# Performance work log

Hardware: AMD Instinct MI355X
Metric: run time of the kernel (lower is better)

The kernel has to match this reference:

```python
import jax, jax.numpy as jnp
import numpy as np

EPS = 1e-8

def squash(t, axis=-1):
    sq = jnp.sum(t * t, axis=axis, keepdims=True)
    scale = sq / (1.0 + sq)
    return scale * t / jnp.sqrt(sq + EPS)

def setup_inputs() -> dict:
    key = jax.random.key(0)
    k1, k2 = jax.random.split(key)
    B, N_IN, D_IN, N_OUT, D_OUT = 256, 1152, 8, 10, 16
    x = jax.random.normal(k1, (B, N_IN, D_IN), dtype=jnp.float32)
    W = 0.01 * jax.random.normal(k2, (1, N_IN, N_OUT, D_OUT, D_IN), dtype=jnp.float32)
    return {"x": x, "W": W}

def reference(x, W):
    # u_hat[b,n,o,j] = sum_i W[0,n,o,j,i] * x[b,n,i]   -> (B, N_in, N_out, D_out)
    u_hat = jnp.einsum('noji,bni->bnoj', W[0], x)
    # b_ij starts with batch dim 1 (as in original torch code) and broadcasts
    b_ij = jnp.zeros((1, u_hat.shape[1], u_hat.shape[2], 1), dtype=u_hat.dtype)
    v_j = None
    for _ in range(3):  # fixed 3 routing iterations
        c_ij = jax.nn.softmax(b_ij, axis=2)            # over output capsules
        s_j = jnp.sum(c_ij * u_hat, axis=1, keepdims=True)  # (B,1,N_out,D_out)
        v_j = squash(s_j, axis=-1)
        b_ij = b_ij + jnp.sum(u_hat * v_j, axis=-1, keepdims=True)
    return jnp.squeeze(v_j, axis=1)  # (B, N_out, D_out)
```

## Files before the change

### kernel.cpp

```cpp
#include <hip/hip_runtime.h>

#define B_ 256
#define N_IN 1152
#define N_OUT 10
#define D_OUT 16
#define OJ 160
#define SN (B_*OJ)
#define LOG2E 1.44269504088896340736f
#define NPB 16
#define NPW 4
#define NSG (N_IN/NPB)
#define NPASSB (NSG*16)

typedef __attribute__((ext_vector_type(8))) short bf16x8;
typedef __attribute__((ext_vector_type(4))) float f32x4;

#define NW_ELEMS (N_IN*N_OUT*D_OUT)
#define NX_ELEMS (B_*N_IN)
#define NWB (NW_ELEMS/256)
#define NTILES ((N_IN/16)*(B_/16))

__device__ __forceinline__ unsigned short f2bf(float f) {
  unsigned u = __float_as_uint(f);
  u += 0x7fffu + ((u >> 16) & 1u);
  return (unsigned short)(u >> 16);
}
__device__ __forceinline__ float bf2f(unsigned short s) {
  return __uint_as_float(((unsigned)s) << 16);
}
__device__ __forceinline__ void split8(const float* p, bf16x8& vh, bf16x8& vl) {
  const float4 a = *(const float4*)p;
  const float4 b = *(const float4*)(p + 4);
  const float w[8] = {a.x,a.y,a.z,a.w,b.x,b.y,b.z,b.w};
#pragma unroll
  for (int e=0;e<8;e++){
    unsigned short hh = f2bf(w[e]);
    vh[e] = (short)hh;
    vl[e] = (short)f2bf(w[e] - bf2f(hh));
  }
}

template<int CTRL>
__device__ __forceinline__ float dpp_add(float xx) {
  int y = __builtin_amdgcn_mov_dpp(__float_as_int(xx), CTRL, 0xF, 0xF, false);
  return xx + __int_as_float(y);
}
__device__ __forceinline__ float row_sum16(float xx) {
  xx = dpp_add<0x128>(xx); xx = dpp_add<0x124>(xx);
  xx = dpp_add<0x122>(xx); xx = dpp_add<0x121>(xx);
  return xx;
}
__device__ __forceinline__ float squash_elem(float t) {
  const float sq = row_sum16(t * t);
  return t * (sq / (1.f + sq)) * rsqrtf(sq + 1e-8f);
}

__device__ __forceinline__ void sgbg_map(int bid, int& sg, int& bg) {
  const int xcd = bid & 7, q = bid >> 3;
  sg = xcd*9 + (q % 9);
  bg = q / 9;
}

__global__ __launch_bounds__(256) void pack_all(const float* __restrict__ W,
                                                const float* __restrict__ x,
                                                short* __restrict__ WH, short* __restrict__ WL,
                                                short* __restrict__ XH, short* __restrict__ XL) {
  const int bid = blockIdx.x, tid = threadIdx.x;
  if (bid < NWB) {
    const int t = bid*256 + tid;
    bf16x8 vh, vl; split8(W + (size_t)t*8, vh, vl);
    ((bf16x8*)WH)[t] = vh; ((bf16x8*)WL)[t] = vl;
  } else {
    __shared__ bf16x8 TH[16*17], TL[16*17];
    const int tile = bid - NWB;
    const int nt = tile >> 4, bt = tile & 15;
    const int nn = tid & 15, bb = tid >> 4;
    bf16x8 vh, vl;
    split8(x + ((size_t)(bt*16+bb)*N_IN + nt*16+nn)*8, vh, vl);
    TH[nn*17 + bb] = vh; TL[nn*17 + bb] = vl;
    __syncthreads();
    const int bb2 = tid & 15, nn2 = tid >> 4;
    const size_t o = (size_t)(nt*16+nn2)*B_ + bt*16 + bb2;
    ((bf16x8*)XH)[o] = TH[nn2*17 + bb2];
    ((bf16x8*)XL)[o] = TL[nn2*17 + bb2];
  }
}


__global__ __launch_bounds__(256) void caps_pass1(const short* __restrict__ WH,
                                                  const short* __restrict__ WL,
                                                  const short* __restrict__ XH,
                                                  const short* __restrict__ XL,
                                                  float* __restrict__ P) {
  __shared__ f32x4 red[3*640];
  int sg, bg; sgbg_map(blockIdx.x, sg, bg);
  const int tid = threadIdx.x, w = tid >> 6, l = tid & 63;
  const int bb = l & 15, c = l >> 4;
  const int b0 = bg * 16;
  const int n0 = sg * NPB + w * NPW;
  const short* Abase = (c & 1)  ? WL : WH;
  const short* Bbase = (c >> 1) ? XL : XH;

  f32x4 acc[N_OUT];
  const f32x4 zz = {0.f,0.f,0.f,0.f};
#pragma unroll
  for (int o=0;o<N_OUT;o++) acc[o] = zz;

  for (int nn=0; nn<NPW; ++nn) {
    const int n = n0 + nn;
    const bf16x8 bfrag = *(const bf16x8*)&Bbase[((size_t)n*B_ + b0 + bb)*8];
    const short* Ap = &Abase[(size_t)n*1280 + bb*8];
#pragma unroll
    for (int o=0;o<N_OUT;o++) {
      const bf16x8 afrag = *(const bf16x8*)&Ap[o*128];
      acc[o] = __builtin_amdgcn_mfma_f32_16x16x32_bf16(afrag, bfrag, acc[o], 0,0,0);
    }
  }

  if (w) {
#pragma unroll
    for (int o=0;o<N_OUT;o++) red[(w-1)*640 + o*64 + l] = acc[o];
  }
  __syncthreads();
  if (!w) {
    float* Pp = &P[(size_t)sg*SN + (size_t)(b0 + bb)*OJ + c*4];
#pragma unroll
    for (int o=0;o<N_OUT;o++) {
      acc[o] += red[o*64+l] + red[640+o*64+l] + red[1280+o*64+l];
      *(f32x4*)&Pp[o*16] = acc[o];
    }
  }
}

__global__ __launch_bounds__(256) void caps_pass23(const short* __restrict__ WH,
                                                   const short* __restrict__ WL,
                                                   const short* __restrict__ XH,
                                                   const short* __restrict__ XL,
                                                   const float* __restrict__ veff,
                                                   float* __restrict__ P) {
  __shared__ f32x4 red[3*640];
  int sg, bg; sgbg_map(blockIdx.x, sg, bg);
  const int tid = threadIdx.x, w = tid >> 6, l = tid & 63;
  const int bb = l & 15, c = l >> 4;
  const int b0 = bg * 16;
  const int n0 = sg * NPB + w * NPW;
  const short* Abase = (c & 1)  ? WL : WH;
  const short* Bbase = (c >> 1) ? XL : XH;

  f32x4 vj[N_OUT], acc[N_OUT];
  const f32x4 zz = {0.f,0.f,0.f,0.f};
  const float* vp = &veff[(size_t)(b0+bb)*OJ + c*4];
#pragma unroll
  for (int o=0;o<N_OUT;o++) { vj[o] = *(const f32x4*)&vp[o*16]; acc[o] = zz; }

  for (int nn=0; nn<NPW; ++nn) {
    const int n = n0 + nn;
    const bf16x8 bfrag = *(const bf16x8*)&Bbase[((size_t)n*B_ + b0 + bb)*8];
    const short* Ap = &Abase[(size_t)n*1280 + bb*8];
    f32x4 u[N_OUT];
#pragma unroll
    for (int o=0;o<N_OUT;o++) {
      const bf16x8 afrag = *(const bf16x8*)&Ap[o*128];
      u[o] = __builtin_amdgcn_mfma_f32_16x16x32_bf16(afrag, bfrag, zz, 0,0,0);
    }
    float ez[N_OUT], Z = 0.f;
#pragma unroll
    for (int o=0;o<N_OUT;o++) {
      float t = u[o][0]*vj[o][0] + u[o][1]*vj[o][1]
              + u[o][2]*vj[o][2] + u[o][3]*vj[o][3];
      t += __shfl_xor(t, 16);
      t += __shfl_xor(t, 32);
      ez[o] = exp2f(t);
      Z += ez[o];
    }
    const float invZ = __builtin_amdgcn_rcpf(Z);
#pragma unroll
    for (int o=0;o<N_OUT;o++) acc[o] += (ez[o] * invZ) * u[o];
  }

  if (w) {
#pragma unroll
    for (int o=0;o<N_OUT;o++) red[(w-1)*640 + o*64 + l] = acc[o];
  }
  __syncthreads();
  if (!w) {
    float* Pp = &P[(size_t)sg*SN + (size_t)(b0 + bb)*OJ + c*4];
#pragma unroll
    for (int o=0;o<N_OUT;o++) {
      acc[o] += red[o*64+l] + red[640+o*64+l] + red[1280+o*64+l];
      *(f32x4*)&Pp[o*16] = acc[o];
    }
  }
}

__global__ __launch_bounds__(256) void caps_finish(const float* __restrict__ P, float scale,
                                                   const float* __restrict__ vprev,
                                                   float* __restrict__ vout, float lscale) {
  const int idx = blockIdx.x*256 + threadIdx.x;
  float t = 0.f;
#pragma unroll 8
  for (int g=0; g<NSG; ++g) t += P[(size_t)g*SN + idx];
  t *= scale;
  float v = squash_elem(t) * lscale;
  if (vprev != nullptr) v += vprev[idx];
  vout[idx] = v;
}

extern "C" void kernel_launch(void* const* d_in, const int* in_sizes, int n_in,
                              void* d_out, int out_size, void* d_ws, size_t ws_size,
                              hipStream_t stream) {
  const float* x = (const float*)d_in[0];
  const float* W = (const float*)d_in[1];
  float* out = (float*)d_out;

  float* P   = (float*)d_ws;
  float* v1  = P  + (size_t)NSG*SN;
  float* v12 = v1 + SN;
  short* WH = (short*)(v12 + SN);
  short* WL = WH + (size_t)NW_ELEMS*8;
  short* XH = WL + (size_t)NW_ELEMS*8;
  short* XL = XH + (size_t)NX_ELEMS*8;

  pack_all<<<NWB + NTILES, 256, 0, stream>>>(W, x, WH, WL, XH, XL);

  caps_pass1<<<NPASSB, 256, 0, stream>>>(WH, WL, XH, XL, P);
  caps_finish<<<SN/256, 256, 0, stream>>>(P, 0.1f, nullptr, v1, LOG2E);

  caps_pass23<<<NPASSB, 256, 0, stream>>>(WH, WL, XH, XL, v1, P);
  caps_finish<<<SN/256, 256, 0, stream>>>(P, 1.0f, v1, v12, LOG2E);

  caps_pass23<<<NPASSB, 256, 0, stream>>>(WH, WL, XH, XL, v12, P);
  caps_finish<<<SN/256, 256, 0, stream>>>(P, 1.0f, nullptr, out, 1.0f);
}
```

Before: 85.88 us.

## Use bf16-only operands in first routing pass and vectorize finish kernel

The first routing pass drops the hi/lo bf16 split compensation. It now uses the MFMA K dimension to cover four input capsules per instruction instead of the four hi/lo cross terms, so each block spans 32 input capsules and writes half as many partial sums. The finish kernel is templated on the partial-group count and processes four elements per thread with float4 loads, and a quad DPP reduction replaces the 16-lane row reduction. In exchange the first-iteration sums lose the low-order correction, which reduces accuracy, and pass1 no longer uses the XCD-aware block mapping.

```diff
diff --git a/kernel.cpp b/kernel.cpp
--- a/kernel.cpp
+++ b/kernel.cpp
@@ -11,6 +11,8 @@
 #define NPW 4
 #define NSG (N_IN/NPB)
 #define NPASSB (NSG*16)
+#define NPB1 32
+#define NSG1 (N_IN/NPB1)
 
 typedef __attribute__((ext_vector_type(8))) short bf16x8;
 typedef __attribute__((ext_vector_type(4))) float f32x4;
@@ -45,14 +47,10 @@
   int y = __builtin_amdgcn_mov_dpp(__float_as_int(xx), CTRL, 0xF, 0xF, false);
   return xx + __int_as_float(y);
 }
-__device__ __forceinline__ float row_sum16(float xx) {
-  xx = dpp_add<0x128>(xx); xx = dpp_add<0x124>(xx);
-  xx = dpp_add<0x122>(xx); xx = dpp_add<0x121>(xx);
+__device__ __forceinline__ float quad_sum4(float xx) {
+  xx = dpp_add<0xB1>(xx);
+  xx = dpp_add<0x4E>(xx);
   return xx;
-}
-__device__ __forceinline__ float squash_elem(float t) {
-  const float sq = row_sum16(t * t);
-  return t * (sq / (1.f + sq)) * rsqrtf(sq + 1e-8f);
 }
 
 __device__ __forceinline__ void sgbg_map(int bid, int& sg, int& bg) {
@@ -86,30 +84,26 @@
   }
 }
 
-
 __global__ __launch_bounds__(256) void caps_pass1(const short* __restrict__ WH,
-                                                  const short* __restrict__ WL,
                                                   const short* __restrict__ XH,
-                                                  const short* __restrict__ XL,
                                                   float* __restrict__ P) {
   __shared__ f32x4 red[3*640];
-  int sg, bg; sgbg_map(blockIdx.x, sg, bg);
   const int tid = threadIdx.x, w = tid >> 6, l = tid & 63;
   const int bb = l & 15, c = l >> 4;
+  const int sg = blockIdx.x, bg = blockIdx.y;
   const int b0 = bg * 16;
-  const int n0 = sg * NPB + w * NPW;
-  const short* Abase = (c & 1)  ? WL : WH;
-  const short* Bbase = (c >> 1) ? XL : XH;
+  const int n0 = sg*NPB1 + w*8;
 
   f32x4 acc[N_OUT];
   const f32x4 zz = {0.f,0.f,0.f,0.f};
 #pragma unroll
   for (int o=0;o<N_OUT;o++) acc[o] = zz;
 
-  for (int nn=0; nn<NPW; ++nn) {
-    const int n = n0 + nn;
-    const bf16x8 bfrag = *(const bf16x8*)&Bbase[((size_t)n*B_ + b0 + bb)*8];
-    const short* Ap = &Abase[(size_t)n*1280 + bb*8];
+#pragma unroll
+  for (int grp=0; grp<2; ++grp) {
+    const int nb = n0 + grp*4 + c;
+    const bf16x8 bfrag = *(const bf16x8*)&XH[((size_t)nb*B_ + b0 + bb)*8];
+    const short* Ap = &WH[(size_t)nb*1280 + bb*8];
 #pragma unroll
     for (int o=0;o<N_OUT;o++) {
       const bf16x8 afrag = *(const bf16x8*)&Ap[o*128];
@@ -193,17 +187,20 @@
   }
 }
 
+template<int GC>
 __global__ __launch_bounds__(256) void caps_finish(const float* __restrict__ P, float scale,
                                                    const float* __restrict__ vprev,
                                                    float* __restrict__ vout, float lscale) {
-  const int idx = blockIdx.x*256 + threadIdx.x;
-  float t = 0.f;
+  const int e0 = (blockIdx.x*256 + threadIdx.x)*4;
+  f32x4 t = {0.f,0.f,0.f,0.f};
 #pragma unroll 8
-  for (int g=0; g<NSG; ++g) t += P[(size_t)g*SN + idx];
+  for (int g=0; g<GC; ++g) t += *(const f32x4*)&P[(size_t)g*SN + e0];
   t *= scale;
-  float v = squash_elem(t) * lscale;
-  if (vprev != nullptr) v += vprev[idx];
-  vout[idx] = v;
+  const float sq = quad_sum4(t[0]*t[0] + t[1]*t[1] + t[2]*t[2] + t[3]*t[3]);
+  const float k = (sq/(1.f+sq)) * rsqrtf(sq + 1e-8f) * lscale;
+  f32x4 v = t * k;
+  if (vprev != nullptr) v += *(const f32x4*)&vprev[e0];
+  *(f32x4*)&vout[e0] = v;
 }
 
 extern "C" void kernel_launch(void* const* d_in, const int* in_sizes, int n_in,
@@ -223,12 +220,12 @@
 
   pack_all<<<NWB + NTILES, 256, 0, stream>>>(W, x, WH, WL, XH, XL);
 
-  caps_pass1<<<NPASSB, 256, 0, stream>>>(WH, WL, XH, XL, P);
-  caps_finish<<<SN/256, 256, 0, stream>>>(P, 0.1f, nullptr, v1, LOG2E);
+  caps_pass1<<<dim3(NSG1,16), 256, 0, stream>>>(WH, XH, P);
+  caps_finish<NSG1><<<SN/1024, 256, 0, stream>>>(P, 0.1f, nullptr, v1, LOG2E);
 
   caps_pass23<<<NPASSB, 256, 0, stream>>>(WH, WL, XH, XL, v1, P);
-  caps_finish<<<SN/256, 256, 0, stream>>>(P, 1.0f, v1, v12, LOG2E);
+  caps_finish<NSG><<<SN/1024, 256, 0, stream>>>(P, 1.0f, v1, v12, LOG2E);
 
   caps_pass23<<<NPASSB, 256, 0, stream>>>(WH, WL, XH, XL, v12, P);
-  caps_finish<<<SN/256, 256, 0, stream>>>(P, 1.0f, nullptr, out, 1.0f);
-}
+  caps_finish<NSG><<<SN/1024, 256, 0, stream>>>(P, 1.0f, nullptr, out, 1.0f);
+}
```

Result: faster. 79.44 us (median of 2 runs) (-7.5%).
